# Kernel tuning notes

Hardware: AMD Instinct MI355X
Metric: run time of the kernel (lower is better)

Reference implementation:

```python
import jax, jax.numpy as jnp
import numpy as np

H = 200          # PREPARED_IMAGE_SIZE
BS = 8
NP = 64          # cloud points
HALF = H / 2.0   # image centre offset (100)


def _project_to_2d(cam_coeffs, points_3d, points_3d_base, points_2d_base):
    # points_3d: (bs, n, 3); cam_coeffs: (bs, 3cams, 2, 3) affine projection
    p3 = points_3d + points_3d_base[:, None]                       # (bs, n, 3)
    p2 = jnp.einsum('bcij,bnj->bcni', cam_coeffs, p3)              # (bs, 3, n, 2)
    return p2 - points_2d_base[:, :, None] + HALF


def _render_points(points, blur_sigmas):
    # points: (bs*3, n, 2) pixel coords; blur_sigmas: (bs, n)
    bs3, n, _ = points.shape
    bs = bs3 // 3
    pts = jnp.clip((points - 100.0) / 100.0, -1.0, 1.0)
    grid = jnp.linspace(-1.0, 1.0, H, dtype=jnp.float32)
    yv, xv = jnp.meshgrid(grid, grid, indexing='ij')
    m = jnp.stack([xv, yv], axis=-1)                               # (H, W, 2)
    diff = m[None, None] - pts[:, :, None, None, :]                # (bs3, n, H, W, 2)
    dst = diff[..., 0] ** 2 + diff[..., 1] ** 2                    # (bs3, n, H, W)
    sig = jnp.repeat(blur_sigmas, 3, axis=0)[:, :, None, None]     # (bs3, n, 1, 1)
    blobs = jnp.exp(-dst / (2.0 * sig ** 2))                       # (bs3, n, H, W)
    masks = jnp.minimum(blobs.sum(axis=1), 1.0)                    # (bs3, H, W)
    sum_ = jnp.maximum(masks.sum(axis=(1, 2), keepdims=True), 1e-8)
    masks_normed = (masks / sum_).reshape(bs, 3, H, H)
    blobs = blobs.reshape(bs, 3, n, H, H)
    return masks_normed, blobs


def setup_inputs() -> dict:
    key = jax.random.key(0)
    ks = jax.random.split(key, 6)
    cam_coeffs = jax.random.normal(ks[0], (BS, 3, 2, 3), dtype=jnp.float32) * 30.0
    cloud_points = jax.random.normal(ks[1], (BS, NP, 3), dtype=jnp.float32)
    masks_target = jax.random.uniform(ks[2], (BS, 3, H, H), dtype=jnp.float32)
    blur_sigmas_cloud = jax.random.uniform(ks[3], (BS, NP), dtype=jnp.float32) * 0.1 + 0.02
    points_3d_base = jax.random.normal(ks[4], (BS, 3), dtype=jnp.float32)
    points_2d_base = jax.random.normal(ks[5], (BS, 3, 2), dtype=jnp.float32)
    return {
        'cam_coeffs': cam_coeffs,
        'cloud_points': cloud_points,
        'masks_target': masks_target,
        'blur_sigmas_cloud': blur_sigmas_cloud,
        'points_3d_base': points_3d_base,
        'points_2d_base': points_2d_base,
    }


def reference(cam_coeffs, cloud_points, masks_target, blur_sigmas_cloud,
              points_3d_base, points_2d_base):
    bs = cam_coeffs.shape[0]
    p2d = _project_to_2d(cam_coeffs, cloud_points, points_3d_base, points_2d_base)
    masks_cloud, blobs = _render_points(p2d.reshape(bs * 3, NP, 2), blur_sigmas_cloud)
    # NOTE: normalization over dims (2,3) = (n_points, H), matching the torch source exactly
    sum_ = jnp.maximum(blobs.sum(axis=(2, 3), keepdims=True), 1e-8)
    blobs_normed = blobs / sum_
    scores = (blobs_normed * masks_target[:, :, None]).sum(axis=(3, 4)).mean(axis=1)
    return masks_cloud, scores
```

## Files before the change

kernel.cpp:

```cpp
#include <hip/hip_runtime.h>

#define H 200
#define NP 64
#define NIMG 24
#define NB 8
#define G 10
#define ROWS 20
#define XH 2
#define XW 100
#define SPI (G*XH)
#define NBLK (NIMG*SPI)
#define GSTEP (2.0f/199.0f)

__global__ __launch_bounds__(256) void prs_main(
    const float* __restrict__ cam,
    const float* __restrict__ cloud,
    const float* __restrict__ mt,
    const float* __restrict__ blur,
    const float* __restrict__ b3,
    const float* __restrict__ b2,
    float* __restrict__ out,
    float* __restrict__ ws_msum,
    float* __restrict__ ws_score)
{
  __shared__ float ex[NP * XW];
  __shared__ float eys[ROWS * NP];
  __shared__ float eyt[NP * ROWS];
  __shared__ float Syp[4 * NP];
  __shared__ float Sy[NP];
  __shared__ float cinv[XW];
  __shared__ float ptx[NP], pty[NP], i2s[NP];
  __shared__ float red[256];

  const int tid = threadIdx.x;
  const int blk = blockIdx.x;
  const int img = blk / SPI;
  const int rem = blk - img * SPI;
  const int strip = rem >> 1;
  const int xh = rem & 1;
  const int b = img / 3;
  const int c = img - b * 3;
  const int ys0 = strip * ROWS;
  const int xb = xh * XW;

  if (tid < NP) {
    int n = tid;
    float p0 = cloud[(b*NP + n)*3 + 0] + b3[b*3 + 0];
    float p1 = cloud[(b*NP + n)*3 + 1] + b3[b*3 + 1];
    float p2 = cloud[(b*NP + n)*3 + 2] + b3[b*3 + 2];
    const float* cc = cam + ((b*3 + c)*2)*3;
    float px = cc[0]*p0 + cc[1]*p1 + cc[2]*p2 - b2[(b*3 + c)*2 + 0];
    float py = cc[3]*p0 + cc[4]*p1 + cc[5]*p2 - b2[(b*3 + c)*2 + 1];
    ptx[n] = fminf(fmaxf(px * 0.01f, -1.0f), 1.0f);
    pty[n] = fminf(fmaxf(py * 0.01f, -1.0f), 1.0f);
    float s = blur[b*NP + n];
    i2s[n] = 1.0f / (2.0f * s * s);
  }
  __syncthreads();

  {
    int n   = tid >> 2;
    int xl0 = (tid & 3) * 25;
    float pxv = ptx[n], iv = i2s[n];
    for (int k = 0; k < 25; ++k) {
      int xl = xl0 + k;
      float dx = (-1.0f + (xb + xl) * GSTEP) - pxv;
      ex[n*XW + xl] = __expf(-dx*dx*iv);
    }
  }
  {
    int n = tid & 63;
    int g = tid >> 6;
    float pyv = pty[n], iv = i2s[n];
    float s = 0.0f;
    for (int y = g*50; y < g*50 + 50; ++y) {
      float dy = (-1.0f + y * GSTEP) - pyv;
      s += __expf(-dy*dy*iv);
    }
    Syp[g*NP + n] = s;
    for (int k = 0; k < 5; ++k) {
      int y = g*5 + k;
      float dy = (-1.0f + (ys0 + y) * GSTEP) - pyv;
      float e = __expf(-dy*dy*iv);
      eys[y*NP + n] = e;
      eyt[n*ROWS + y] = e;
    }
  }
  __syncthreads();
  if (tid < NP) Sy[tid] = Syp[tid] + Syp[NP + tid] + Syp[2*NP + tid] + Syp[3*NP + tid];
  __syncthreads();
  if (tid < XW) {
    float s = 0.0f;
    for (int n = 0; n < NP; ++n) s += ex[n*XW + tid] * Sy[n];
    cinv[tid] = 1.0f / fmaxf(s, 1e-8f);
  }
  __syncthreads();

  float msl = 0.0f;
  if (tid < 128) {
    if (tid < 125) {
      int yg = tid / 25;
      int xg = tid - yg * 25;
      int x0 = xg * 4, y0 = yg * 4;
      float acc[4][4];
      #pragma unroll
      for (int i = 0; i < 4; ++i)
        #pragma unroll
        for (int j = 0; j < 4; ++j) acc[i][j] = 0.0f;
      for (int n = 0; n < NP; ++n) {
        float4 exv = *(float4*)&ex[n*XW + x0];
        float4 eyv = *(float4*)&eyt[n*ROWS + y0];
        acc[0][0] += eyv.x*exv.x; acc[0][1] += eyv.x*exv.y; acc[0][2] += eyv.x*exv.z; acc[0][3] += eyv.x*exv.w;
        acc[1][0] += eyv.y*exv.x; acc[1][1] += eyv.y*exv.y; acc[1][2] += eyv.y*exv.z; acc[1][3] += eyv.y*exv.w;
        acc[2][0] += eyv.z*exv.x; acc[2][1] += eyv.z*exv.y; acc[2][2] += eyv.z*exv.z; acc[2][3] += eyv.z*exv.w;
        acc[3][0] += eyv.w*exv.x; acc[3][1] += eyv.w*exv.y; acc[3][2] += eyv.w*exv.z; acc[3][3] += eyv.w*exv.w;
      }
      #pragma unroll
      for (int i = 0; i < 4; ++i) {
        float4 v;
        v.x = fminf(acc[i][0], 1.0f);
        v.y = fminf(acc[i][1], 1.0f);
        v.z = fminf(acc[i][2], 1.0f);
        v.w = fminf(acc[i][3], 1.0f);
        msl += v.x + v.y + v.z + v.w;
        *(float4*)&out[img*(H*H) + (ys0 + y0 + i)*H + xb + x0] = v;
      }
    }
  } else {
    int st = tid - 128;
    int ng = st >> 3;
    int xt = st & 7;
    int n0 = ng * 4;
    float sacc[4] = {0.0f, 0.0f, 0.0f, 0.0f};
    for (int xq = xt; xq < 25; xq += 8) {
      int xl0 = xq * 4;
      float t[4][4];
      #pragma unroll
      for (int i = 0; i < 4; ++i)
        #pragma unroll
        for (int j = 0; j < 4; ++j) t[i][j] = 0.0f;
      for (int y = 0; y < ROWS; ++y) {
        float4 eyv = *(float4*)&eys[y*NP + n0];
        float4 mv  = *(const float4*)&mt[img*(H*H) + (ys0 + y)*H + xb + xl0];
        t[0][0] += eyv.x*mv.x; t[0][1] += eyv.x*mv.y; t[0][2] += eyv.x*mv.z; t[0][3] += eyv.x*mv.w;
        t[1][0] += eyv.y*mv.x; t[1][1] += eyv.y*mv.y; t[1][2] += eyv.y*mv.z; t[1][3] += eyv.y*mv.w;
        t[2][0] += eyv.z*mv.x; t[2][1] += eyv.z*mv.y; t[2][2] += eyv.z*mv.z; t[2][3] += eyv.z*mv.w;
        t[3][0] += eyv.w*mv.x; t[3][1] += eyv.w*mv.y; t[3][2] += eyv.w*mv.z; t[3][3] += eyv.w*mv.w;
      }
      float4 cv = *(float4*)&cinv[xl0];
      #pragma unroll
      for (int i = 0; i < 4; ++i) {
        float4 exv = *(float4*)&ex[(n0 + i)*XW + xl0];
        sacc[i] += t[i][0]*exv.x*cv.x + t[i][1]*exv.y*cv.y
                 + t[i][2]*exv.z*cv.z + t[i][3]*exv.w*cv.w;
      }
    }
    #pragma unroll
    for (int off = 4; off > 0; off >>= 1) {
      #pragma unroll
      for (int i = 0; i < 4; ++i) sacc[i] += __shfl_down(sacc[i], off, 8);
    }
    if (xt == 0) {
      #pragma unroll
      for (int i = 0; i < 4; ++i) ws_score[blk*NP + n0 + i] = sacc[i];
    }
  }

  red[tid] = msl;
  __syncthreads();
  #pragma unroll
  for (int s = 128; s > 0; s >>= 1) {
    if (tid < s) red[tid] += red[tid + s];
    __syncthreads();
  }
  if (tid == 0) ws_msum[blk] = red[0];
}

__global__ __launch_bounds__(256) void prs_finish(
    float* __restrict__ out,
    const float* __restrict__ ws_msum,
    const float* __restrict__ ws_score)
{
  const int blk = blockIdx.x;
  const int tid = threadIdx.x;
  if (blk < NBLK) {
    const int img = blk / SPI;
    const int rem = blk - img * SPI;
    const int strip = rem >> 1;
    const int xh = rem & 1;
    __shared__ float invs;
    if (tid == 0) {
      float s = 0.0f;
      for (int i = 0; i < SPI; ++i) s += ws_msum[img*SPI + i];
      invs = 1.0f / fmaxf(s, 1e-8f);
    }
    __syncthreads();
    const float inv = invs;
    for (int q = tid; q < 500; q += 256) {
      int ry = q / 25;
      int rx = q - ry * 25;
      float* p = out + img*(H*H) + (strip*ROWS + ry)*H + xh*XW + rx*4;
      float4 v = *(float4*)p;
      v.x *= inv; v.y *= inv; v.z *= inv; v.w *= inv;
      *(float4*)p = v;
    }
  } else {
    const int bb = blk - NBLK;
    if (tid < NP) {
      float s = 0.0f;
      for (int cc = 0; cc < 3; ++cc)
        for (int sh = 0; sh < SPI; ++sh)
          s += ws_score[(((bb*3 + cc)*SPI) + sh)*NP + tid];
      out[NIMG*(H*H) + bb*NP + tid] = s * (1.0f/3.0f);
    }
  }
}

extern "C" void kernel_launch(void* const* d_in, const int* in_sizes, int n_in,
                              void* d_out, int out_size, void* d_ws, size_t ws_size,
                              hipStream_t stream) {
  const float* cam   = (const float*)d_in[0];
  const float* cloud = (const float*)d_in[1];
  const float* mt    = (const float*)d_in[2];
  const float* blur  = (const float*)d_in[3];
  const float* b3    = (const float*)d_in[4];
  const float* b2    = (const float*)d_in[5];
  float* out = (float*)d_out;

  float* ws_msum  = (float*)d_ws;
  float* ws_score = ws_msum + 512;

  prs_main<<<NBLK, 256, 0, stream>>>(cam, cloud, mt, blur, b3, b2,
                                     out, ws_msum, ws_score);
  prs_finish<<<NBLK + NB, 256, 0, stream>>>(out, ws_msum, ws_score);
}
```

Baseline: 20.23 us.

## Use packed fp16 dot2 for mask and score contractions with staged target tile

Both inner contractions (mask rendering over points, score over rows) now convert the separable Gaussian factors and the target tile to packed half2 and accumulate with v_dot2 fp16→fp32 instructions. The target mask tile is staged once into shared memory as row-pair packs, so it is no longer re-read from global inside the score loop. The aim is to halve FMA instruction count and cut global loads, but it adds several packing passes plus another barrier phase and loses precision in the exponential factors.

```diff
diff --git a/kernel.cpp b/kernel.cpp
--- a/kernel.cpp
+++ b/kernel.cpp
@@ -4,13 +4,32 @@
 #define NP 64
 #define NIMG 24
 #define NB 8
-#define G 10
-#define ROWS 20
-#define XH 2
-#define XW 100
-#define SPI (G*XH)
-#define NBLK (NIMG*SPI)
+#define NPIX (H*H)
 #define GSTEP (2.0f/199.0f)
+#define SPI 20
+#define NWORK (NIMG*SPI)
+
+typedef __fp16 h2 __attribute__((ext_vector_type(2)));
+
+__device__ __forceinline__ float fdot2f(unsigned int a, unsigned int b, float c) {
+  h2 ha = __builtin_bit_cast(h2, a);
+  h2 hb = __builtin_bit_cast(h2, b);
+#if __has_builtin(__builtin_amdgcn_fdot2)
+  return __builtin_amdgcn_fdot2(ha, hb, c, false);
+#else
+  return c + (float)ha.x * (float)hb.x + (float)ha.y * (float)hb.y;
+#endif
+}
+
+__device__ __forceinline__ unsigned int pk2(float lo, float hi) {
+#if __has_builtin(__builtin_amdgcn_cvt_pkrtz)
+  h2 h = __builtin_amdgcn_cvt_pkrtz(lo, hi);
+  return __builtin_bit_cast(unsigned int, h);
+#else
+  h2 h; h.x = (__fp16)lo; h.y = (__fp16)hi;
+  return __builtin_bit_cast(unsigned int, h);
+#endif
+}
 
 __global__ __launch_bounds__(256) void prs_main(
     const float* __restrict__ cam,
@@ -21,14 +40,16 @@
     const float* __restrict__ b2,
     float* __restrict__ out,
     float* __restrict__ ws_msum,
-    float* __restrict__ ws_score)
+    float* __restrict__ ws_scr)
 {
-  __shared__ float ex[NP * XW];
-  __shared__ float eys[ROWS * NP];
-  __shared__ float eyt[NP * ROWS];
-  __shared__ float Syp[4 * NP];
+  __shared__ float ex[NP*100];
+  __shared__ float eys[20*NP];
+  __shared__ unsigned int exp2_[32*100];
+  __shared__ unsigned int eyp2[32*20];
+  __shared__ unsigned int eyy[NP*12];
+  __shared__ unsigned int Mp[100*12];
+  __shared__ float cinv[100];
   __shared__ float Sy[NP];
-  __shared__ float cinv[XW];
   __shared__ float ptx[NP], pty[NP], i2s[NP];
   __shared__ float red[256];
 
@@ -39,9 +60,9 @@
   const int strip = rem >> 1;
   const int xh = rem & 1;
   const int b = img / 3;
-  const int c = img - b * 3;
-  const int ys0 = strip * ROWS;
-  const int xb = xh * XW;
+  const int c = img - 3 * b;
+  const int ys0 = strip * 20;
+  const int xb = xh * 100;
 
   if (tid < NP) {
     int n = tid;
@@ -58,40 +79,52 @@
   }
   __syncthreads();
 
+  for (int e = tid; e < 20*NP; e += 256) {
+    int y = e >> 6, n = e & 63;
+    float d = (-1.0f + (ys0 + y)*GSTEP) - pty[n];
+    eys[y*NP + n] = __expf(-d*d*i2s[n]);
+  }
+  for (int e = tid; e < NP*100; e += 256) {
+    int n = e / 100, x = e - n*100;
+    float d = (-1.0f + (xb + x)*GSTEP) - ptx[n];
+    ex[n*100 + x] = __expf(-d*d*i2s[n]);
+  }
   {
-    int n   = tid >> 2;
-    int xl0 = (tid & 3) * 25;
-    float pxv = ptx[n], iv = i2s[n];
-    for (int k = 0; k < 25; ++k) {
-      int xl = xl0 + k;
-      float dx = (-1.0f + (xb + xl) * GSTEP) - pxv;
-      ex[n*XW + xl] = __expf(-dx*dx*iv);
-    }
-  }
-  {
-    int n = tid & 63;
-    int g = tid >> 6;
+    int n = tid & 63, g = tid >> 6;
     float pyv = pty[n], iv = i2s[n];
     float s = 0.0f;
     for (int y = g*50; y < g*50 + 50; ++y) {
-      float dy = (-1.0f + y * GSTEP) - pyv;
-      s += __expf(-dy*dy*iv);
-    }
-    Syp[g*NP + n] = s;
-    for (int k = 0; k < 5; ++k) {
-      int y = g*5 + k;
-      float dy = (-1.0f + (ys0 + y) * GSTEP) - pyv;
-      float e = __expf(-dy*dy*iv);
-      eys[y*NP + n] = e;
-      eyt[n*ROWS + y] = e;
-    }
-  }
-  __syncthreads();
-  if (tid < NP) Sy[tid] = Syp[tid] + Syp[NP + tid] + Syp[2*NP + tid] + Syp[3*NP + tid];
-  __syncthreads();
-  if (tid < XW) {
+      float d = (-1.0f + y*GSTEP) - pyv;
+      s += __expf(-d*d*iv);
+    }
+    red[g*NP + n] = s;
+  }
+  __syncthreads();
+
+  for (int e = tid; e < 3200; e += 256) {
+    int n2 = e / 100, x = e - n2*100;
+    exp2_[n2*100 + x] = pk2(ex[(2*n2)*100 + x], ex[(2*n2+1)*100 + x]);
+  }
+  for (int e = tid; e < 640; e += 256) {
+    int n2 = e / 20, y = e - n2*20;
+    eyp2[n2*20 + y] = pk2(eys[y*NP + 2*n2], eys[y*NP + 2*n2 + 1]);
+  }
+  for (int e = tid; e < 640; e += 256) {
+    int n = e / 10, y2 = e - n*10;
+    eyy[n*12 + y2] = pk2(eys[(2*y2)*NP + n], eys[(2*y2+1)*NP + n]);
+  }
+  for (int e = tid; e < 1000; e += 256) {
+    int y2 = e / 100, x = e - y2*100;
+    const float* mb = mt + img*NPIX + (ys0 + 2*y2)*H + xb + x;
+    Mp[x*12 + y2] = pk2(mb[0], mb[H]);
+  }
+  if (tid < NP)
+    Sy[tid] = red[tid] + red[NP + tid] + red[2*NP + tid] + red[3*NP + tid];
+  __syncthreads();
+
+  if (tid < 100) {
     float s = 0.0f;
-    for (int n = 0; n < NP; ++n) s += ex[n*XW + tid] * Sy[n];
+    for (int n = 0; n < NP; ++n) s += ex[n*100 + tid] * Sy[n];
     cinv[tid] = 1.0f / fmaxf(s, 1e-8f);
   }
   __syncthreads();
@@ -100,21 +133,26 @@
   if (tid < 128) {
     if (tid < 125) {
       int yg = tid / 25;
-      int xg = tid - yg * 25;
-      int x0 = xg * 4, y0 = yg * 4;
+      int xg = tid - yg*25;
+      int x0 = xg*4, y0 = yg*4;
       float acc[4][4];
       #pragma unroll
       for (int i = 0; i < 4; ++i)
         #pragma unroll
         for (int j = 0; j < 4; ++j) acc[i][j] = 0.0f;
-      for (int n = 0; n < NP; ++n) {
-        float4 exv = *(float4*)&ex[n*XW + x0];
-        float4 eyv = *(float4*)&eyt[n*ROWS + y0];
-        acc[0][0] += eyv.x*exv.x; acc[0][1] += eyv.x*exv.y; acc[0][2] += eyv.x*exv.z; acc[0][3] += eyv.x*exv.w;
-        acc[1][0] += eyv.y*exv.x; acc[1][1] += eyv.y*exv.y; acc[1][2] += eyv.y*exv.z; acc[1][3] += eyv.y*exv.w;
-        acc[2][0] += eyv.z*exv.x; acc[2][1] += eyv.z*exv.y; acc[2][2] += eyv.z*exv.z; acc[2][3] += eyv.z*exv.w;
-        acc[3][0] += eyv.w*exv.x; acc[3][1] += eyv.w*exv.y; acc[3][2] += eyv.w*exv.z; acc[3][3] += eyv.w*exv.w;
+      for (int n2 = 0; n2 < 32; ++n2) {
+        uint4 eyv = *(uint4*)&eyp2[n2*20 + y0];
+        uint4 exv = *(uint4*)&exp2_[n2*100 + x0];
+        acc[0][0]=fdot2f(eyv.x,exv.x,acc[0][0]); acc[0][1]=fdot2f(eyv.x,exv.y,acc[0][1]);
+        acc[0][2]=fdot2f(eyv.x,exv.z,acc[0][2]); acc[0][3]=fdot2f(eyv.x,exv.w,acc[0][3]);
+        acc[1][0]=fdot2f(eyv.y,exv.x,acc[1][0]); acc[1][1]=fdot2f(eyv.y,exv.y,acc[1][1]);
+        acc[1][2]=fdot2f(eyv.y,exv.z,acc[1][2]); acc[1][3]=fdot2f(eyv.y,exv.w,acc[1][3]);
+        acc[2][0]=fdot2f(eyv.z,exv.x,acc[2][0]); acc[2][1]=fdot2f(eyv.z,exv.y,acc[2][1]);
+        acc[2][2]=fdot2f(eyv.z,exv.z,acc[2][2]); acc[2][3]=fdot2f(eyv.z,exv.w,acc[2][3]);
+        acc[3][0]=fdot2f(eyv.w,exv.x,acc[3][0]); acc[3][1]=fdot2f(eyv.w,exv.y,acc[3][1]);
+        acc[3][2]=fdot2f(eyv.w,exv.z,acc[3][2]); acc[3][3]=fdot2f(eyv.w,exv.w,acc[3][3]);
       }
+      float* ob = out + img*NPIX;
       #pragma unroll
       for (int i = 0; i < 4; ++i) {
         float4 v;
@@ -123,7 +161,7 @@
         v.z = fminf(acc[i][2], 1.0f);
         v.w = fminf(acc[i][3], 1.0f);
         msl += v.x + v.y + v.z + v.w;
-        *(float4*)&out[img*(H*H) + (ys0 + y0 + i)*H + xb + x0] = v;
+        *(float4*)&ob[(ys0 + y0 + i)*H + xb + x0] = v;
       }
     }
   } else {
@@ -131,28 +169,30 @@
     int ng = st >> 3;
     int xt = st & 7;
     int n0 = ng * 4;
+    uint4 ea[4], eb4[4]; uint2 ec[4];
+    #pragma unroll
+    for (int i = 0; i < 4; ++i) {
+      const unsigned int* p = &eyy[(n0 + i)*12];
+      ea[i]  = *(const uint4*)p;
+      eb4[i] = *(const uint4*)(p + 4);
+      ec[i]  = *(const uint2*)(p + 8);
+    }
     float sacc[4] = {0.0f, 0.0f, 0.0f, 0.0f};
-    for (int xq = xt; xq < 25; xq += 8) {
-      int xl0 = xq * 4;
-      float t[4][4];
-      #pragma unroll
-      for (int i = 0; i < 4; ++i)
-        #pragma unroll
-        for (int j = 0; j < 4; ++j) t[i][j] = 0.0f;
-      for (int y = 0; y < ROWS; ++y) {
-        float4 eyv = *(float4*)&eys[y*NP + n0];
-        float4 mv  = *(const float4*)&mt[img*(H*H) + (ys0 + y)*H + xb + xl0];
-        t[0][0] += eyv.x*mv.x; t[0][1] += eyv.x*mv.y; t[0][2] += eyv.x*mv.z; t[0][3] += eyv.x*mv.w;
-        t[1][0] += eyv.y*mv.x; t[1][1] += eyv.y*mv.y; t[1][2] += eyv.y*mv.z; t[1][3] += eyv.y*mv.w;
-        t[2][0] += eyv.z*mv.x; t[2][1] += eyv.z*mv.y; t[2][2] += eyv.z*mv.z; t[2][3] += eyv.z*mv.w;
-        t[3][0] += eyv.w*mv.x; t[3][1] += eyv.w*mv.y; t[3][2] += eyv.w*mv.z; t[3][3] += eyv.w*mv.w;
-      }
-      float4 cv = *(float4*)&cinv[xl0];
+    for (int x = xt; x < 100; x += 8) {
+      const unsigned int* q = &Mp[x*12];
+      uint4 ma = *(const uint4*)q;
+      uint4 mb = *(const uint4*)(q + 4);
+      uint2 mc = *(const uint2*)(q + 8);
+      float cvx = cinv[x];
       #pragma unroll
       for (int i = 0; i < 4; ++i) {
-        float4 exv = *(float4*)&ex[(n0 + i)*XW + xl0];
-        sacc[i] += t[i][0]*exv.x*cv.x + t[i][1]*exv.y*cv.y
-                 + t[i][2]*exv.z*cv.z + t[i][3]*exv.w*cv.w;
+        float t = 0.0f;
+        t = fdot2f(ea[i].x, ma.x, t);  t = fdot2f(ea[i].y, ma.y, t);
+        t = fdot2f(ea[i].z, ma.z, t);  t = fdot2f(ea[i].w, ma.w, t);
+        t = fdot2f(eb4[i].x, mb.x, t); t = fdot2f(eb4[i].y, mb.y, t);
+        t = fdot2f(eb4[i].z, mb.z, t); t = fdot2f(eb4[i].w, mb.w, t);
+        t = fdot2f(ec[i].x, mc.x, t);  t = fdot2f(ec[i].y, mc.y, t);
+        sacc[i] += t * ex[(n0 + i)*100 + x] * cvx;
       }
     }
     #pragma unroll
@@ -162,7 +202,7 @@
     }
     if (xt == 0) {
       #pragma unroll
-      for (int i = 0; i < 4; ++i) ws_score[blk*NP + n0 + i] = sacc[i];
+      for (int i = 0; i < 4; ++i) ws_scr[blk*NP + n0 + i] = sacc[i];
     }
   }
 
@@ -179,11 +219,11 @@
 __global__ __launch_bounds__(256) void prs_finish(
     float* __restrict__ out,
     const float* __restrict__ ws_msum,
-    const float* __restrict__ ws_score)
+    const float* __restrict__ ws_scr)
 {
   const int blk = blockIdx.x;
   const int tid = threadIdx.x;
-  if (blk < NBLK) {
+  if (blk < NWORK) {
     const int img = blk / SPI;
     const int rem = blk - img * SPI;
     const int strip = rem >> 1;
@@ -199,19 +239,19 @@
     for (int q = tid; q < 500; q += 256) {
       int ry = q / 25;
       int rx = q - ry * 25;
-      float* p = out + img*(H*H) + (strip*ROWS + ry)*H + xh*XW + rx*4;
+      float* p = out + img*NPIX + (strip*20 + ry)*H + xh*100 + rx*4;
       float4 v = *(float4*)p;
       v.x *= inv; v.y *= inv; v.z *= inv; v.w *= inv;
       *(float4*)p = v;
     }
   } else {
-    const int bb = blk - NBLK;
+    const int bb = blk - NWORK;
     if (tid < NP) {
       float s = 0.0f;
       for (int cc = 0; cc < 3; ++cc)
         for (int sh = 0; sh < SPI; ++sh)
-          s += ws_score[(((bb*3 + cc)*SPI) + sh)*NP + tid];
-      out[NIMG*(H*H) + bb*NP + tid] = s * (1.0f/3.0f);
+          s += ws_scr[((bb*3 + cc)*SPI + sh)*NP + tid];
+      out[NIMG*NPIX + bb*NP + tid] = s * (1.0f/3.0f);
     }
   }
 }
@@ -227,10 +267,10 @@
   const float* b2    = (const float*)d_in[5];
   float* out = (float*)d_out;
 
-  float* ws_msum  = (float*)d_ws;
-  float* ws_score = ws_msum + 512;
-
-  prs_main<<<NBLK, 256, 0, stream>>>(cam, cloud, mt, blur, b3, b2,
-                                     out, ws_msum, ws_score);
-  prs_finish<<<NBLK + NB, 256, 0, stream>>>(out, ws_msum, ws_score);
-}
+  float* ws_msum = (float*)d_ws;
+  float* ws_scr  = ws_msum + 512;
+
+  prs_main<<<NWORK, 256, 0, stream>>>(cam, cloud, mt, blur, b3, b2,
+                                      out, ws_msum, ws_scr);
+  prs_finish<<<NWORK + NB, 256, 0, stream>>>(out, ws_msum, ws_scr);
+}
```

New measurement: 20.73 us. 2.5% more time.
